# Optimization experiments

Measured on AMD Instinct MI355X. Metric: run time of the kernel, lower is better.

Reference implementation:

```python
import jax, jax.numpy as jnp
import numpy as np

HID = 64

def _lstm_layer(x_seq, h0, c0, w_ih, w_hh, b_ih, b_hh):
    # x_seq: [B,T,I]; PyTorch gate order: i, f, g, o
    x_proj = jnp.einsum('bti,gi->btg', x_seq, w_ih) + b_ih  # [B,T,4H]
    x_proj = jnp.swapaxes(x_proj, 0, 1)                      # [T,B,4H]

    def step(carry, xp):
        h, c = carry
        gates = xp + h @ w_hh.T + b_hh
        i, f, g, o = jnp.split(gates, 4, axis=-1)
        c_new = jax.nn.sigmoid(f) * c + jax.nn.sigmoid(i) * jnp.tanh(g)
        h_new = jax.nn.sigmoid(o) * jnp.tanh(c_new)
        return (h_new, c_new), h_new

    (hT, cT), hs = jax.lax.scan(step, (h0, c0), x_proj)
    return jnp.swapaxes(hs, 0, 1), hT, cT  # [B,T,H]


def setup_inputs() -> dict:
    key = jax.random.key(0)
    ks = jax.random.split(key, 12)
    B, T, I = 1024, 512, 5
    s = 1.0 / np.sqrt(HID)
    u = lambda k, shape: jax.random.uniform(k, shape, jnp.float32, -s, s)
    return {
        'x': jax.random.normal(ks[0], (B, T, I), jnp.float32),
        'h0': jnp.zeros((2, B, HID), jnp.float32),
        'c0': jnp.zeros((2, B, HID), jnp.float32),
        'w_ih0': u(ks[1], (4 * HID, I)),
        'w_hh0': u(ks[2], (4 * HID, HID)),
        'b_ih0': u(ks[3], (4 * HID,)),
        'b_hh0': u(ks[4], (4 * HID,)),
        'w_ih1': u(ks[5], (4 * HID, HID)),
        'w_hh1': u(ks[6], (4 * HID, HID)),
        'b_ih1': u(ks[7], (4 * HID,)),
        'b_hh1': u(ks[8], (4 * HID,)),
        'w_mean': u(ks[9], (1, HID)),
        'b_mean': u(ks[10], (1,)),
        'w_critic': u(ks[11], (1, HID)),
        'b_critic': jnp.zeros((1,), jnp.float32),
    }


def reference(x, h0, c0, w_ih0, w_hh0, b_ih0, b_hh0,
              w_ih1, w_hh1, b_ih1, b_hh1,
              w_mean, b_mean, w_critic, b_critic):
    out0, _, _ = _lstm_layer(x, h0[0], c0[0], w_ih0, w_hh0, b_ih0, b_hh0)
    out1, _, _ = _lstm_layer(out0, h0[1], c0[1], w_ih1, w_hh1, b_ih1, b_hh1)
    last = out1[:, -1, :]                       # [B,H]
    mean_lin = last @ w_mean.T + b_mean         # [B,1]
    mean = 2.0 * jnp.tanh(mean_lin)
    log_std = jax.nn.softplus(mean_lin)         # source bug: reuses actor_mean_fc
    state_value = last @ w_critic.T + b_critic  # [B,1]
    return mean, log_std, state_value
```

## Files before the change

kernel.cpp:

```cpp
#include <hip/hip_runtime.h>
#include <math.h>

#define NB    256
#define NT    512
#define ROWS  4
#define B_TOT 1024
#define T_TOT 512
#define HROW  104
#define XT    32

typedef _Float16 f16;
typedef _Float16 f16x8 __attribute__((ext_vector_type(8)));
typedef float    f32x4 __attribute__((ext_vector_type(4)));

__device__ __forceinline__ float rcp_f(float v){ return __builtin_amdgcn_rcpf(v); }
__device__ __forceinline__ float sig_f(float x){ return rcp_f(1.0f + __expf(-x)); }
__device__ __forceinline__ float tanh_f(float x){ return 1.0f - 2.0f*rcp_f(__expf(2.0f*x) + 1.0f); }

#define MFMA16(a,b,c) __builtin_amdgcn_mfma_f32_16x16x32_f16((a),(b),(c),0,0,0)

__global__ __launch_bounds__(NT, 2) void lstm_pipe(
    const float* __restrict__ x,
    const float* __restrict__ h0i, const float* __restrict__ c0i,
    const float* __restrict__ wih0, const float* __restrict__ whh0,
    const float* __restrict__ bih0, const float* __restrict__ bhh0,
    const float* __restrict__ wih1, const float* __restrict__ whh1,
    const float* __restrict__ bih1, const float* __restrict__ bhh1,
    const float* __restrict__ wmean, const float* __restrict__ bmean,
    const float* __restrict__ wcrit, const float* __restrict__ bcrit,
    float* __restrict__ out)
{
    const int tid  = threadIdx.x;
    const int lane = tid & 63;
    const int wv   = tid >> 6;
    const bool isX = (wv < 4);
    const int ug   = wv & 3;
    const int l15  = lane & 15;
    const int kgrp = lane >> 4;
    const int r0   = blockIdx.x * ROWS;
    const int uloc = lane >> 2;
    const int bb   = lane & 3;

    __shared__ __align__(16) f16 hbuf[2][16][HROW];
    __shared__ __align__(16) f16 ybuf[2][16][HROW];
    __shared__ float xt[ROWS][XT][5];
    __shared__ __align__(16) float gbuf[8][4][4][16];

    f16x8 aX[4][3];
    f16x8 aY[4][4];
    float bpk[4];
    float cOwn;

    if (isX){
#pragma unroll
        for (int q = 0; q < 4; ++q){
            const int gr = q*64 + ug*16 + l15;
#pragma unroll
            for (int c2 = 0; c2 < 2; ++c2){
                const float* pw = whh0 + (size_t)gr*64 + c2*32 + kgrp*8;
                f16x8 v;
#pragma unroll
                for (int j = 0; j < 8; ++j) v[j] = (f16)pw[j];
                aX[q][c2] = v;
            }
            {
                f16x8 v;
#pragma unroll
                for (int j = 0; j < 8; ++j){
                    int k = kgrp*8 + j;
                    v[j] = (k < 5) ? (f16)wih0[gr*5 + k] : (f16)0.f;
                }
                aX[q][2] = v;
            }
            const int gu = q*64 + ug*16 + uloc;
            bpk[q] = bih0[gu] + bhh0[gu];
        }
        cOwn = c0i[(size_t)(r0+bb)*64 + ug*16 + uloc];
    } else {
#pragma unroll
        for (int q = 0; q < 4; ++q){
            const int gr = q*64 + ug*16 + l15;
#pragma unroll
            for (int c2 = 0; c2 < 2; ++c2){
                const float* pw = wih1 + (size_t)gr*64 + c2*32 + kgrp*8;
                const float* qw = whh1 + (size_t)gr*64 + c2*32 + kgrp*8;
                f16x8 v, u2;
#pragma unroll
                for (int j = 0; j < 8; ++j){ v[j] = (f16)pw[j]; u2[j] = (f16)qw[j]; }
                aY[q][c2]   = v;
                aY[q][2+c2] = u2;
            }
            const int gu = q*64 + ug*16 + uloc;
            bpk[q] = bih1[gu] + bhh1[gu];
        }
        cOwn = c0i[(size_t)B_TOT*64 + (size_t)(r0+bb)*64 + ug*16 + uloc];
    }

    for (int e = tid; e < 2*16*HROW; e += NT){
        ((f16*)hbuf)[e] = (f16)0.f;
        ((f16*)ybuf)[e] = (f16)0.f;
    }
    __syncthreads();
    if (tid < ROWS*64){
        int cc = tid >> 6, u = tid & 63;
        hbuf[0][cc][u] = (f16)h0i[(size_t)(r0+cc)*64 + u];
        ybuf[1][cc][u] = (f16)h0i[(size_t)B_TOT*64 + (size_t)(r0+cc)*64 + u];
    }
    if (tid < ROWS*5){
        int cc = tid/5, i = tid - cc*5;
        hbuf[0][cc][64+i] = (f16)x[(size_t)(r0+cc)*T_TOT*5 + i];
    }
    for (int e = tid; e < ROWS*XT*5; e += NT){
        int r = e/160, rem = e - r*160, ts = rem/5, i = rem - ts*5;
        xt[r][ts][i] = x[((size_t)(r0+r)*T_TOT + ts)*5 + i];
    }
    __syncthreads();

#pragma unroll 1
    for (int t = 0; t <= T_TOT; ++t){
        const int p = t & 1;

        if ((t+1) < T_TOT && ((t+1) & 31) == 0){
            for (int e = tid; e < ROWS*XT*5; e += NT){
                int r = e/160, rem = e - r*160, ts = rem/5, i = rem - ts*5;
                xt[r][ts][i] = x[((size_t)(r0+r)*T_TOT + (t+1+ts))*5 + i];
            }
            __syncthreads();
        }
        if ((t+1) < T_TOT && tid < ROWS*5){
            int cc = tid/5, i = tid - cc*5;
            hbuf[p^1][cc][64+i] = (f16)xt[cc][(t+1)&31][i];
        }

        if (isX){ if (t < T_TOT){
            const f16* bp = &hbuf[p][l15][kgrp*8];
            f16x8 b0 = *(const f16x8*)(bp);
            f16x8 b1 = *(const f16x8*)(bp + 32);
            f16x8 b2 = *(const f16x8*)(bp + 64);
#pragma unroll
            for (int q = 0; q < 4; ++q){
                f32x4 a = {0.f,0.f,0.f,0.f};
                a = MFMA16(aX[q][0], b0, a);
                a = MFMA16(aX[q][1], b1, a);
                a = MFMA16(aX[q][2], b2, a);
                if (l15 < ROWS) *(f32x4*)&gbuf[wv][q][l15][kgrp*4] = a;
            }
            float ii = gbuf[wv][0][bb][uloc] + bpk[0];
            float ff = gbuf[wv][1][bb][uloc] + bpk[1];
            float gg = gbuf[wv][2][bb][uloc] + bpk[2];
            float oo = gbuf[wv][3][bb][uloc] + bpk[3];
            cOwn = sig_f(ff)*cOwn + sig_f(ii)*tanh_f(gg);
            hbuf[p^1][bb][ug*16 + uloc] = (f16)(sig_f(oo)*tanh_f(cOwn));
        }} else { if (t >= 1){
            const f16* hp = &hbuf[p][l15][kgrp*8];
            f16x8 b0 = *(const f16x8*)(hp);
            f16x8 b1 = *(const f16x8*)(hp + 32);
            const f16* yp = &ybuf[p][l15][kgrp*8];
            f16x8 b2 = *(const f16x8*)(yp);
            f16x8 b3 = *(const f16x8*)(yp + 32);
#pragma unroll
            for (int q = 0; q < 4; ++q){
                f32x4 a = {0.f,0.f,0.f,0.f};
                a = MFMA16(aY[q][0], b0, a);
                a = MFMA16(aY[q][1], b1, a);
                a = MFMA16(aY[q][2], b2, a);
                a = MFMA16(aY[q][3], b3, a);
                if (l15 < ROWS) *(f32x4*)&gbuf[wv][q][l15][kgrp*4] = a;
            }
            float ii = gbuf[wv][0][bb][uloc] + bpk[0];
            float ff = gbuf[wv][1][bb][uloc] + bpk[1];
            float gg = gbuf[wv][2][bb][uloc] + bpk[2];
            float oo = gbuf[wv][3][bb][uloc] + bpk[3];
            cOwn = sig_f(ff)*cOwn + sig_f(ii)*tanh_f(gg);
            ybuf[p^1][bb][ug*16 + uloc] = (f16)(sig_f(oo)*tanh_f(cOwn));
        }}
        __syncthreads();
    }

    if (wv < ROWS){
        const int cc = wv, u = lane;
        float hr = (float)ybuf[1][cc][u];
        float pm = hr * wmean[u];
        float pc = hr * wcrit[u];
#pragma unroll
        for (int o = 32; o > 0; o >>= 1){
            pm += __shfl_down(pm, o);
            pc += __shfl_down(pc, o);
        }
        if (u == 0){
            float m = pm + bmean[0];
            out[r0+cc]           = 2.f*tanh_f(m);
            out[B_TOT + r0+cc]   = __logf(1.f + __expf(m));
            out[2*B_TOT + r0+cc] = pc + bcrit[0];
        }
    }
}

extern "C" void kernel_launch(void* const* d_in, const int* in_sizes, int n_in,
                              void* d_out, int out_size, void* d_ws, size_t ws_size,
                              hipStream_t stream) {
    const float* x     = (const float*)d_in[0];
    const float* h0i   = (const float*)d_in[1];
    const float* c0i   = (const float*)d_in[2];
    const float* wih0  = (const float*)d_in[3];
    const float* whh0  = (const float*)d_in[4];
    const float* bih0  = (const float*)d_in[5];
    const float* bhh0  = (const float*)d_in[6];
    const float* wih1  = (const float*)d_in[7];
    const float* whh1  = (const float*)d_in[8];
    const float* bih1  = (const float*)d_in[9];
    const float* bhh1  = (const float*)d_in[10];
    const float* wmean = (const float*)d_in[11];
    const float* bmean = (const float*)d_in[12];
    const float* wcrit = (const float*)d_in[13];
    const float* bcrit = (const float*)d_in[14];

    lstm_pipe<<<NB, NT, 0, stream>>>(x, h0i, c0i, wih0, whh0, bih0, bhh0,
                                     wih1, whh1, bih1, bhh1,
                                     wmean, bmean, wcrit, bcrit,
                                     (float*)d_out);
}
```

Baseline: 350.5 us.

## Transpose MFMA operands and redistribute gates via shuffles instead of LDS

Swaps the MFMA operand roles so the hidden state becomes the A operand and weights the B operand, which puts batch rows on the output's row axis and hidden units on its columns. Each lane can then collect its four gate values with cross-lane shuffles from the accumulator rather than writing them to a shared-memory staging buffer and reading them back. The bias is folded into the accumulator initialisation. This removes an LDS round trip per gate per timestep on the serial critical path, at the cost of 16 shuffles plus selects per step.

```diff
diff --git a/kernel.cpp b/kernel.cpp
--- a/kernel.cpp
+++ b/kernel.cpp
@@ -19,7 +19,7 @@
 
 #define MFMA16(a,b,c) __builtin_amdgcn_mfma_f32_16x16x32_f16((a),(b),(c),0,0,0)
 
-__global__ __launch_bounds__(NT, 2) void lstm_pipe(
+__global__ __launch_bounds__(NT, 2) void lstm_tr(
     const float* __restrict__ x,
     const float* __restrict__ h0i, const float* __restrict__ c0i,
     const float* __restrict__ wih0, const float* __restrict__ whh0,
@@ -38,30 +38,27 @@
     const int l15  = lane & 15;
     const int kgrp = lane >> 4;
     const int r0   = blockIdx.x * ROWS;
-    const int uloc = lane >> 2;
-    const int bb   = lane & 3;
+    const int un   = ug*16 + l15;
 
     __shared__ __align__(16) f16 hbuf[2][16][HROW];
     __shared__ __align__(16) f16 ybuf[2][16][HROW];
     __shared__ float xt[ROWS][XT][5];
-    __shared__ __align__(16) float gbuf[8][4][4][16];
-
-    f16x8 aX[4][3];
-    f16x8 aY[4][4];
-    float bpk[4];
+
+    f16x8 bfr[4][4];
+    float bq[4];
     float cOwn;
 
     if (isX){
 #pragma unroll
         for (int q = 0; q < 4; ++q){
-            const int gr = q*64 + ug*16 + l15;
+            const int gr = q*64 + un;
 #pragma unroll
             for (int c2 = 0; c2 < 2; ++c2){
                 const float* pw = whh0 + (size_t)gr*64 + c2*32 + kgrp*8;
                 f16x8 v;
 #pragma unroll
                 for (int j = 0; j < 8; ++j) v[j] = (f16)pw[j];
-                aX[q][c2] = v;
+                bfr[q][c2] = v;
             }
             {
                 f16x8 v;
@@ -70,16 +67,16 @@
                     int k = kgrp*8 + j;
                     v[j] = (k < 5) ? (f16)wih0[gr*5 + k] : (f16)0.f;
                 }
-                aX[q][2] = v;
-            }
-            const int gu = q*64 + ug*16 + uloc;
-            bpk[q] = bih0[gu] + bhh0[gu];
-        }
-        cOwn = c0i[(size_t)(r0+bb)*64 + ug*16 + uloc];
+                bfr[q][2] = v;
+            }
+            bfr[q][3] = (f16x8)(f16)0.f;
+            bq[q] = bih0[gr] + bhh0[gr];
+        }
+        cOwn = c0i[(size_t)(r0+kgrp)*64 + un];
     } else {
 #pragma unroll
         for (int q = 0; q < 4; ++q){
-            const int gr = q*64 + ug*16 + l15;
+            const int gr = q*64 + un;
 #pragma unroll
             for (int c2 = 0; c2 < 2; ++c2){
                 const float* pw = wih1 + (size_t)gr*64 + c2*32 + kgrp*8;
@@ -87,13 +84,12 @@
                 f16x8 v, u2;
 #pragma unroll
                 for (int j = 0; j < 8; ++j){ v[j] = (f16)pw[j]; u2[j] = (f16)qw[j]; }
-                aY[q][c2]   = v;
-                aY[q][2+c2] = u2;
-            }
-            const int gu = q*64 + ug*16 + uloc;
-            bpk[q] = bih1[gu] + bhh1[gu];
-        }
-        cOwn = c0i[(size_t)B_TOT*64 + (size_t)(r0+bb)*64 + ug*16 + uloc];
+                bfr[q][c2]   = v;
+                bfr[q][2+c2] = u2;
+            }
+            bq[q] = bih1[gr] + bhh1[gr];
+        }
+        cOwn = c0i[(size_t)B_TOT*64 + (size_t)(r0+kgrp)*64 + un];
     }
 
     for (int e = tid; e < 2*16*HROW; e += NT){
@@ -111,7 +107,7 @@
         hbuf[0][cc][64+i] = (f16)x[(size_t)(r0+cc)*T_TOT*5 + i];
     }
     for (int e = tid; e < ROWS*XT*5; e += NT){
-        int r = e/160, rem = e - r*160, ts = rem/5, i = rem - ts*5;
+        int r = e/(XT*5), rem = e - r*(XT*5), ts = rem/5, i = rem - ts*5;
         xt[r][ts][i] = x[((size_t)(r0+r)*T_TOT + ts)*5 + i];
     }
     __syncthreads();
@@ -122,7 +118,7 @@
 
         if ((t+1) < T_TOT && ((t+1) & 31) == 0){
             for (int e = tid; e < ROWS*XT*5; e += NT){
-                int r = e/160, rem = e - r*160, ts = rem/5, i = rem - ts*5;
+                int r = e/(XT*5), rem = e - r*(XT*5), ts = rem/5, i = rem - ts*5;
                 xt[r][ts][i] = x[((size_t)(r0+r)*T_TOT + (t+1+ts))*5 + i];
             }
             __syncthreads();
@@ -133,46 +129,60 @@
         }
 
         if (isX){ if (t < T_TOT){
-            const f16* bp = &hbuf[p][l15][kgrp*8];
-            f16x8 b0 = *(const f16x8*)(bp);
-            f16x8 b1 = *(const f16x8*)(bp + 32);
-            f16x8 b2 = *(const f16x8*)(bp + 64);
-#pragma unroll
-            for (int q = 0; q < 4; ++q){
-                f32x4 a = {0.f,0.f,0.f,0.f};
-                a = MFMA16(aX[q][0], b0, a);
-                a = MFMA16(aX[q][1], b1, a);
-                a = MFMA16(aX[q][2], b2, a);
-                if (l15 < ROWS) *(f32x4*)&gbuf[wv][q][l15][kgrp*4] = a;
-            }
-            float ii = gbuf[wv][0][bb][uloc] + bpk[0];
-            float ff = gbuf[wv][1][bb][uloc] + bpk[1];
-            float gg = gbuf[wv][2][bb][uloc] + bpk[2];
-            float oo = gbuf[wv][3][bb][uloc] + bpk[3];
-            cOwn = sig_f(ff)*cOwn + sig_f(ii)*tanh_f(gg);
-            hbuf[p^1][bb][ug*16 + uloc] = (f16)(sig_f(oo)*tanh_f(cOwn));
+            const f16* ap = &hbuf[p][l15][kgrp*8];
+            f16x8 a0 = *(const f16x8*)(ap);
+            f16x8 a1 = *(const f16x8*)(ap + 32);
+            f16x8 a2 = *(const f16x8*)(ap + 64);
+            f32x4 ac[4];
+#pragma unroll
+            for (int q = 0; q < 4; ++q){
+                f32x4 a = {bq[q], bq[q], bq[q], bq[q]};
+                a = MFMA16(a0, bfr[q][0], a);
+                a = MFMA16(a1, bfr[q][1], a);
+                a = MFMA16(a2, bfr[q][2], a);
+                ac[q] = a;
+            }
+            float g[4];
+#pragma unroll
+            for (int q = 0; q < 4; ++q){
+                float t0 = __shfl(ac[q][0], l15);
+                float t1 = __shfl(ac[q][1], l15);
+                float t2 = __shfl(ac[q][2], l15);
+                float t3 = __shfl(ac[q][3], l15);
+                g[q] = (kgrp==0) ? t0 : (kgrp==1) ? t1 : (kgrp==2) ? t2 : t3;
+            }
+            cOwn = sig_f(g[1])*cOwn + sig_f(g[0])*tanh_f(g[2]);
+            float hn = sig_f(g[3])*tanh_f(cOwn);
+            hbuf[p^1][kgrp][un] = (f16)hn;
         }} else { if (t >= 1){
             const f16* hp = &hbuf[p][l15][kgrp*8];
-            f16x8 b0 = *(const f16x8*)(hp);
-            f16x8 b1 = *(const f16x8*)(hp + 32);
+            f16x8 a0 = *(const f16x8*)(hp);
+            f16x8 a1 = *(const f16x8*)(hp + 32);
             const f16* yp = &ybuf[p][l15][kgrp*8];
-            f16x8 b2 = *(const f16x8*)(yp);
-            f16x8 b3 = *(const f16x8*)(yp + 32);
-#pragma unroll
-            for (int q = 0; q < 4; ++q){
-                f32x4 a = {0.f,0.f,0.f,0.f};
-                a = MFMA16(aY[q][0], b0, a);
-                a = MFMA16(aY[q][1], b1, a);
-                a = MFMA16(aY[q][2], b2, a);
-                a = MFMA16(aY[q][3], b3, a);
-                if (l15 < ROWS) *(f32x4*)&gbuf[wv][q][l15][kgrp*4] = a;
-            }
-            float ii = gbuf[wv][0][bb][uloc] + bpk[0];
-            float ff = gbuf[wv][1][bb][uloc] + bpk[1];
-            float gg = gbuf[wv][2][bb][uloc] + bpk[2];
-            float oo = gbuf[wv][3][bb][uloc] + bpk[3];
-            cOwn = sig_f(ff)*cOwn + sig_f(ii)*tanh_f(gg);
-            ybuf[p^1][bb][ug*16 + uloc] = (f16)(sig_f(oo)*tanh_f(cOwn));
+            f16x8 a2 = *(const f16x8*)(yp);
+            f16x8 a3 = *(const f16x8*)(yp + 32);
+            f32x4 ac[4];
+#pragma unroll
+            for (int q = 0; q < 4; ++q){
+                f32x4 a = {bq[q], bq[q], bq[q], bq[q]};
+                a = MFMA16(a0, bfr[q][0], a);
+                a = MFMA16(a1, bfr[q][1], a);
+                a = MFMA16(a2, bfr[q][2], a);
+                a = MFMA16(a3, bfr[q][3], a);
+                ac[q] = a;
+            }
+            float g[4];
+#pragma unroll
+            for (int q = 0; q < 4; ++q){
+                float t0 = __shfl(ac[q][0], l15);
+                float t1 = __shfl(ac[q][1], l15);
+                float t2 = __shfl(ac[q][2], l15);
+                float t3 = __shfl(ac[q][3], l15);
+                g[q] = (kgrp==0) ? t0 : (kgrp==1) ? t1 : (kgrp==2) ? t2 : t3;
+            }
+            cOwn = sig_f(g[1])*cOwn + sig_f(g[0])*tanh_f(g[2]);
+            float hn = sig_f(g[3])*tanh_f(cOwn);
+            ybuf[p^1][kgrp][un] = (f16)hn;
         }}
         __syncthreads();
     }
@@ -215,8 +225,8 @@
     const float* wcrit = (const float*)d_in[13];
     const float* bcrit = (const float*)d_in[14];
 
-    lstm_pipe<<<NB, NT, 0, stream>>>(x, h0i, c0i, wih0, whh0, bih0, bhh0,
-                                     wih1, whh1, bih1, bhh1,
-                                     wmean, bmean, wcrit, bcrit,
-                                     (float*)d_out);
+    lstm_tr<<<NB, NT, 0, stream>>>(x, h0i, c0i, wih0, whh0, bih0, bhh0,
+                                   wih1, whh1, bih1, bhh1,
+                                   wmean, bmean, wcrit, bcrit,
+                                   (float*)d_out);
 }
```

Measured after the change: 390.8 us. +11.5%, slower.

## Halve block to four waves, each wave computing two unit groups

Applied to the files above, without the earlier changes.

The block shrinks from eight waves to four. Each wave now holds weight fragments for two 16-unit groups and computes both gate sets sequentially, which halves the threads taking part in each per-step barrier. Wave priority is raised around the recurrent compute. The cost is twice the serial MFMA and activation work per wave on the critical path of each timestep, plus doubled register pressure for the weight fragments.

```diff
diff --git a/kernel.cpp b/kernel.cpp
--- a/kernel.cpp
+++ b/kernel.cpp
@@ -2,7 +2,7 @@
 #include <math.h>
 
 #define NB    256
-#define NT    512
+#define NT    256
 #define ROWS  4
 #define B_TOT 1024
 #define T_TOT 512
@@ -19,7 +19,7 @@
 
 #define MFMA16(a,b,c) __builtin_amdgcn_mfma_f32_16x16x32_f16((a),(b),(c),0,0,0)
 
-__global__ __launch_bounds__(NT, 2) void lstm_pipe(
+__global__ __launch_bounds__(NT, 2) void lstm_pipe2(
     const float* __restrict__ x,
     const float* __restrict__ h0i, const float* __restrict__ c0i,
     const float* __restrict__ wih0, const float* __restrict__ whh0,
@@ -33,8 +33,8 @@
     const int tid  = threadIdx.x;
     const int lane = tid & 63;
     const int wv   = tid >> 6;
-    const bool isX = (wv < 4);
-    const int ug   = wv & 3;
+    const bool isX = (wv < 2);
+    const int wq   = wv & 1;
     const int l15  = lane & 15;
     const int kgrp = lane >> 4;
     const int r0   = blockIdx.x * ROWS;
@@ -44,56 +44,64 @@
     __shared__ __align__(16) f16 hbuf[2][16][HROW];
     __shared__ __align__(16) f16 ybuf[2][16][HROW];
     __shared__ float xt[ROWS][XT][5];
-    __shared__ __align__(16) float gbuf[8][4][4][16];
-
-    f16x8 aX[4][3];
-    f16x8 aY[4][4];
-    float bpk[4];
-    float cOwn;
+    __shared__ __align__(16) float gbuf[4][2][4][ROWS][16];
+
+    f16x8 afr[2][4][4];
+    float bpk[2][4];
+    float cOwn[2];
 
     if (isX){
 #pragma unroll
-        for (int q = 0; q < 4; ++q){
-            const int gr = q*64 + ug*16 + l15;
-#pragma unroll
-            for (int c2 = 0; c2 < 2; ++c2){
-                const float* pw = whh0 + (size_t)gr*64 + c2*32 + kgrp*8;
-                f16x8 v;
-#pragma unroll
-                for (int j = 0; j < 8; ++j) v[j] = (f16)pw[j];
-                aX[q][c2] = v;
-            }
-            {
-                f16x8 v;
-#pragma unroll
-                for (int j = 0; j < 8; ++j){
-                    int k = kgrp*8 + j;
-                    v[j] = (k < 5) ? (f16)wih0[gr*5 + k] : (f16)0.f;
-                }
-                aX[q][2] = v;
-            }
-            const int gu = q*64 + ug*16 + uloc;
-            bpk[q] = bih0[gu] + bhh0[gu];
-        }
-        cOwn = c0i[(size_t)(r0+bb)*64 + ug*16 + uloc];
+        for (int sg = 0; sg < 2; ++sg){
+            const int ug = 2*wq + sg;
+#pragma unroll
+            for (int q = 0; q < 4; ++q){
+                const int gr = q*64 + ug*16 + l15;
+#pragma unroll
+                for (int c2 = 0; c2 < 2; ++c2){
+                    const float* pw = whh0 + (size_t)gr*64 + c2*32 + kgrp*8;
+                    f16x8 v;
+#pragma unroll
+                    for (int j = 0; j < 8; ++j) v[j] = (f16)pw[j];
+                    afr[sg][q][c2] = v;
+                }
+                {
+                    f16x8 v;
+#pragma unroll
+                    for (int j = 0; j < 8; ++j){
+                        int k = kgrp*8 + j;
+                        v[j] = (k < 5) ? (f16)wih0[gr*5 + k] : (f16)0.f;
+                    }
+                    afr[sg][q][2] = v;
+                }
+                afr[sg][q][3] = (f16x8)(f16)0.f;
+                const int gu = q*64 + ug*16 + uloc;
+                bpk[sg][q] = bih0[gu] + bhh0[gu];
+            }
+            cOwn[sg] = c0i[(size_t)(r0 + bb)*64 + ug*16 + uloc];
+        }
     } else {
 #pragma unroll
-        for (int q = 0; q < 4; ++q){
-            const int gr = q*64 + ug*16 + l15;
-#pragma unroll
-            for (int c2 = 0; c2 < 2; ++c2){
-                const float* pw = wih1 + (size_t)gr*64 + c2*32 + kgrp*8;
-                const float* qw = whh1 + (size_t)gr*64 + c2*32 + kgrp*8;
-                f16x8 v, u2;
-#pragma unroll
-                for (int j = 0; j < 8; ++j){ v[j] = (f16)pw[j]; u2[j] = (f16)qw[j]; }
-                aY[q][c2]   = v;
-                aY[q][2+c2] = u2;
-            }
-            const int gu = q*64 + ug*16 + uloc;
-            bpk[q] = bih1[gu] + bhh1[gu];
-        }
-        cOwn = c0i[(size_t)B_TOT*64 + (size_t)(r0+bb)*64 + ug*16 + uloc];
+        for (int sg = 0; sg < 2; ++sg){
+            const int ug = 2*wq + sg;
+#pragma unroll
+            for (int q = 0; q < 4; ++q){
+                const int gr = q*64 + ug*16 + l15;
+#pragma unroll
+                for (int c2 = 0; c2 < 2; ++c2){
+                    const float* pw = wih1 + (size_t)gr*64 + c2*32 + kgrp*8;
+                    const float* qw = whh1 + (size_t)gr*64 + c2*32 + kgrp*8;
+                    f16x8 v, u2;
+#pragma unroll
+                    for (int j = 0; j < 8; ++j){ v[j] = (f16)pw[j]; u2[j] = (f16)qw[j]; }
+                    afr[sg][q][c2]   = v;
+                    afr[sg][q][2+c2] = u2;
+                }
+                const int gu = q*64 + ug*16 + uloc;
+                bpk[sg][q] = bih1[gu] + bhh1[gu];
+            }
+            cOwn[sg] = c0i[(size_t)B_TOT*64 + (size_t)(r0 + bb)*64 + ug*16 + uloc];
+        }
     }
 
     for (int e = tid; e < 2*16*HROW; e += NT){
@@ -111,7 +119,7 @@
         hbuf[0][cc][64+i] = (f16)x[(size_t)(r0+cc)*T_TOT*5 + i];
     }
     for (int e = tid; e < ROWS*XT*5; e += NT){
-        int r = e/160, rem = e - r*160, ts = rem/5, i = rem - ts*5;
+        int r = e/(XT*5), rem = e - r*(XT*5), ts = rem/5, i = rem - ts*5;
         xt[r][ts][i] = x[((size_t)(r0+r)*T_TOT + ts)*5 + i];
     }
     __syncthreads();
@@ -122,7 +130,7 @@
 
         if ((t+1) < T_TOT && ((t+1) & 31) == 0){
             for (int e = tid; e < ROWS*XT*5; e += NT){
-                int r = e/160, rem = e - r*160, ts = rem/5, i = rem - ts*5;
+                int r = e/(XT*5), rem = e - r*(XT*5), ts = rem/5, i = rem - ts*5;
                 xt[r][ts][i] = x[((size_t)(r0+r)*T_TOT + (t+1+ts))*5 + i];
             }
             __syncthreads();
@@ -133,46 +141,56 @@
         }
 
         if (isX){ if (t < T_TOT){
+            __builtin_amdgcn_s_setprio(1);
             const f16* bp = &hbuf[p][l15][kgrp*8];
             f16x8 b0 = *(const f16x8*)(bp);
             f16x8 b1 = *(const f16x8*)(bp + 32);
             f16x8 b2 = *(const f16x8*)(bp + 64);
 #pragma unroll
-            for (int q = 0; q < 4; ++q){
-                f32x4 a = {0.f,0.f,0.f,0.f};
-                a = MFMA16(aX[q][0], b0, a);
-                a = MFMA16(aX[q][1], b1, a);
-                a = MFMA16(aX[q][2], b2, a);
-                if (l15 < ROWS) *(f32x4*)&gbuf[wv][q][l15][kgrp*4] = a;
-            }
-            float ii = gbuf[wv][0][bb][uloc] + bpk[0];
-            float ff = gbuf[wv][1][bb][uloc] + bpk[1];
-            float gg = gbuf[wv][2][bb][uloc] + bpk[2];
-            float oo = gbuf[wv][3][bb][uloc] + bpk[3];
-            cOwn = sig_f(ff)*cOwn + sig_f(ii)*tanh_f(gg);
-            hbuf[p^1][bb][ug*16 + uloc] = (f16)(sig_f(oo)*tanh_f(cOwn));
+            for (int sg = 0; sg < 2; ++sg){
+#pragma unroll
+                for (int q = 0; q < 4; ++q){
+                    f32x4 a = {0.f,0.f,0.f,0.f};
+                    a = MFMA16(afr[sg][q][0], b0, a);
+                    a = MFMA16(afr[sg][q][1], b1, a);
+                    a = MFMA16(afr[sg][q][2], b2, a);
+                    if (l15 < ROWS) *(f32x4*)&gbuf[wv][sg][q][l15][kgrp*4] = a;
+                }
+                float gi = gbuf[wv][sg][0][bb][uloc] + bpk[sg][0];
+                float gf = gbuf[wv][sg][1][bb][uloc] + bpk[sg][1];
+                float gg = gbuf[wv][sg][2][bb][uloc] + bpk[sg][2];
+                float go = gbuf[wv][sg][3][bb][uloc] + bpk[sg][3];
+                cOwn[sg] = sig_f(gf)*cOwn[sg] + sig_f(gi)*tanh_f(gg);
+                hbuf[p^1][bb][(2*wq+sg)*16 + uloc] = (f16)(sig_f(go)*tanh_f(cOwn[sg]));
+            }
+            __builtin_amdgcn_s_setprio(0);
         }} else { if (t >= 1){
+            __builtin_amdgcn_s_setprio(1);
             const f16* hp = &hbuf[p][l15][kgrp*8];
             f16x8 b0 = *(const f16x8*)(hp);
             f16x8 b1 = *(const f16x8*)(hp + 32);
             const f16* yp = &ybuf[p][l15][kgrp*8];
-            f16x8 b2 = *(const f16x8*)(yp);
-            f16x8 b3 = *(const f16x8*)(yp + 32);
-#pragma unroll
-            for (int q = 0; q < 4; ++q){
-                f32x4 a = {0.f,0.f,0.f,0.f};
-                a = MFMA16(aY[q][0], b0, a);
-                a = MFMA16(aY[q][1], b1, a);
-                a = MFMA16(aY[q][2], b2, a);
-                a = MFMA16(aY[q][3], b3, a);
-                if (l15 < ROWS) *(f32x4*)&gbuf[wv][q][l15][kgrp*4] = a;
-            }
-            float ii = gbuf[wv][0][bb][uloc] + bpk[0];
-            float ff = gbuf[wv][1][bb][uloc] + bpk[1];
-            float gg = gbuf[wv][2][bb][uloc] + bpk[2];
-            float oo = gbuf[wv][3][bb][uloc] + bpk[3];
-            cOwn = sig_f(ff)*cOwn + sig_f(ii)*tanh_f(gg);
-            ybuf[p^1][bb][ug*16 + uloc] = (f16)(sig_f(oo)*tanh_f(cOwn));
+            f16x8 y0 = *(const f16x8*)(yp);
+            f16x8 y1 = *(const f16x8*)(yp + 32);
+#pragma unroll
+            for (int sg = 0; sg < 2; ++sg){
+#pragma unroll
+                for (int q = 0; q < 4; ++q){
+                    f32x4 a = {0.f,0.f,0.f,0.f};
+                    a = MFMA16(afr[sg][q][0], b0, a);
+                    a = MFMA16(afr[sg][q][1], b1, a);
+                    a = MFMA16(afr[sg][q][2], y0, a);
+                    a = MFMA16(afr[sg][q][3], y1, a);
+                    if (l15 < ROWS) *(f32x4*)&gbuf[wv][sg][q][l15][kgrp*4] = a;
+                }
+                float gi = gbuf[wv][sg][0][bb][uloc] + bpk[sg][0];
+                float gf = gbuf[wv][sg][1][bb][uloc] + bpk[sg][1];
+                float gg = gbuf[wv][sg][2][bb][uloc] + bpk[sg][2];
+                float go = gbuf[wv][sg][3][bb][uloc] + bpk[sg][3];
+                cOwn[sg] = sig_f(gf)*cOwn[sg] + sig_f(gi)*tanh_f(gg);
+                ybuf[p^1][bb][(2*wq+sg)*16 + uloc] = (f16)(sig_f(go)*tanh_f(cOwn[sg]));
+            }
+            __builtin_amdgcn_s_setprio(0);
         }}
         __syncthreads();
     }
@@ -215,8 +233,8 @@
     const float* wcrit = (const float*)d_in[13];
     const float* bcrit = (const float*)d_in[14];
 
-    lstm_pipe<<<NB, NT, 0, stream>>>(x, h0i, c0i, wih0, whh0, bih0, bhh0,
-                                     wih1, whh1, bih1, bhh1,
-                                     wmean, bmean, wcrit, bcrit,
-                                     (float*)d_out);
+    lstm_pipe2<<<NB, NT, 0, stream>>>(x, h0i, c0i, wih0, whh0, bih0, bhh0,
+                                      wih1, whh1, bih1, bhh1,
+                                      wmean, bmean, wcrit, bcrit,
+                                      (float*)d_out);
 }
```

Result: slower. 465.3 us (+32.7%).

## Redistribute gate rows so DPP row-shares replace LDS gate exchange

Applied to the files above, without the earlier changes.

Reorders the MFMA A-operand rows so that the four gates for each (batch,unit) pair sit in the same 16-lane row group. A thread can then collect its i/f/g/o values with DPP row_share moves instead of writing accumulators to a shared gbuf and reading them back. Biases are folded into the MFMA accumulator init, and s_setprio brackets the recurrent step. The goal is to remove an LDS round trip and its wait from the serial per-timestep critical path, at the cost of extra DPP moves and selects.

```diff
diff --git a/kernel.cpp b/kernel.cpp
--- a/kernel.cpp
+++ b/kernel.cpp
@@ -17,9 +17,15 @@
 __device__ __forceinline__ float sig_f(float x){ return rcp_f(1.0f + __expf(-x)); }
 __device__ __forceinline__ float tanh_f(float x){ return 1.0f - 2.0f*rcp_f(__expf(2.0f*x) + 1.0f); }
 
+template<int CTRL>
+__device__ __forceinline__ float dpp_mov(float v){
+    int r = __builtin_amdgcn_update_dpp(0, __float_as_int(v), CTRL, 0xF, 0xF, false);
+    return __int_as_float(r);
+}
+
 #define MFMA16(a,b,c) __builtin_amdgcn_mfma_f32_16x16x32_f16((a),(b),(c),0,0,0)
 
-__global__ __launch_bounds__(NT, 2) void lstm_pipe(
+__global__ __launch_bounds__(NT, 2) void lstm_dpp(
     const float* __restrict__ x,
     const float* __restrict__ h0i, const float* __restrict__ c0i,
     const float* __restrict__ wih0, const float* __restrict__ whh0,
@@ -34,34 +40,35 @@
     const int lane = tid & 63;
     const int wv   = tid >> 6;
     const bool isX = (wv < 4);
-    const int ug   = wv & 3;
+    const int w    = wv & 3;
     const int l15  = lane & 15;
     const int kgrp = lane >> 4;
     const int r0   = blockIdx.x * ROWS;
-    const int uloc = lane >> 2;
-    const int bb   = lane & 3;
+    const int gA   = l15 & 3;
+    const int usA  = l15 >> 2;
+    const int grp  = l15 >> 2;
+    const int bown = l15 & 3;
+    const int uown = 16*w + 4*grp + kgrp;
 
     __shared__ __align__(16) f16 hbuf[2][16][HROW];
     __shared__ __align__(16) f16 ybuf[2][16][HROW];
     __shared__ float xt[ROWS][XT][5];
-    __shared__ __align__(16) float gbuf[8][4][4][16];
-
-    f16x8 aX[4][3];
-    f16x8 aY[4][4];
-    float bpk[4];
+
+    f16x8 afr[4][4];
+    f32x4 bv[4];
     float cOwn;
 
     if (isX){
 #pragma unroll
-        for (int q = 0; q < 4; ++q){
-            const int gr = q*64 + ug*16 + l15;
+        for (int s = 0; s < 4; ++s){
+            const int gr = gA*64 + 16*w + 4*s + usA;
 #pragma unroll
             for (int c2 = 0; c2 < 2; ++c2){
                 const float* pw = whh0 + (size_t)gr*64 + c2*32 + kgrp*8;
                 f16x8 v;
 #pragma unroll
                 for (int j = 0; j < 8; ++j) v[j] = (f16)pw[j];
-                aX[q][c2] = v;
+                afr[s][c2] = v;
             }
             {
                 f16x8 v;
@@ -70,16 +77,20 @@
                     int k = kgrp*8 + j;
                     v[j] = (k < 5) ? (f16)wih0[gr*5 + k] : (f16)0.f;
                 }
-                aX[q][2] = v;
-            }
-            const int gu = q*64 + ug*16 + uloc;
-            bpk[q] = bih0[gu] + bhh0[gu];
-        }
-        cOwn = c0i[(size_t)(r0+bb)*64 + ug*16 + uloc];
+                afr[s][2] = v;
+            }
+            afr[s][3] = (f16x8)(f16)0.f;
+            const int us = 16*w + 4*s + kgrp;
+            f32x4 bb;
+#pragma unroll
+            for (int r = 0; r < 4; ++r) bb[r] = bih0[r*64 + us] + bhh0[r*64 + us];
+            bv[s] = bb;
+        }
+        cOwn = c0i[(size_t)(r0 + bown)*64 + uown];
     } else {
 #pragma unroll
-        for (int q = 0; q < 4; ++q){
-            const int gr = q*64 + ug*16 + l15;
+        for (int s = 0; s < 4; ++s){
+            const int gr = gA*64 + 16*w + 4*s + usA;
 #pragma unroll
             for (int c2 = 0; c2 < 2; ++c2){
                 const float* pw = wih1 + (size_t)gr*64 + c2*32 + kgrp*8;
@@ -87,13 +98,16 @@
                 f16x8 v, u2;
 #pragma unroll
                 for (int j = 0; j < 8; ++j){ v[j] = (f16)pw[j]; u2[j] = (f16)qw[j]; }
-                aY[q][c2]   = v;
-                aY[q][2+c2] = u2;
-            }
-            const int gu = q*64 + ug*16 + uloc;
-            bpk[q] = bih1[gu] + bhh1[gu];
-        }
-        cOwn = c0i[(size_t)B_TOT*64 + (size_t)(r0+bb)*64 + ug*16 + uloc];
+                afr[s][c2]   = v;
+                afr[s][2+c2] = u2;
+            }
+            const int us = 16*w + 4*s + kgrp;
+            f32x4 bb;
+#pragma unroll
+            for (int r = 0; r < 4; ++r) bb[r] = bih1[r*64 + us] + bhh1[r*64 + us];
+            bv[s] = bb;
+        }
+        cOwn = c0i[(size_t)B_TOT*64 + (size_t)(r0 + bown)*64 + uown];
     }
 
     for (int e = tid; e < 2*16*HROW; e += NT){
@@ -111,7 +125,7 @@
         hbuf[0][cc][64+i] = (f16)x[(size_t)(r0+cc)*T_TOT*5 + i];
     }
     for (int e = tid; e < ROWS*XT*5; e += NT){
-        int r = e/160, rem = e - r*160, ts = rem/5, i = rem - ts*5;
+        int r = e/(XT*5), rem = e - r*(XT*5), ts = rem/5, i = rem - ts*5;
         xt[r][ts][i] = x[((size_t)(r0+r)*T_TOT + ts)*5 + i];
     }
     __syncthreads();
@@ -122,7 +136,7 @@
 
         if ((t+1) < T_TOT && ((t+1) & 31) == 0){
             for (int e = tid; e < ROWS*XT*5; e += NT){
-                int r = e/160, rem = e - r*160, ts = rem/5, i = rem - ts*5;
+                int r = e/(XT*5), rem = e - r*(XT*5), ts = rem/5, i = rem - ts*5;
                 xt[r][ts][i] = x[((size_t)(r0+r)*T_TOT + (t+1+ts))*5 + i];
             }
             __syncthreads();
@@ -133,46 +147,61 @@
         }
 
         if (isX){ if (t < T_TOT){
+            __builtin_amdgcn_s_setprio(1);
             const f16* bp = &hbuf[p][l15][kgrp*8];
             f16x8 b0 = *(const f16x8*)(bp);
             f16x8 b1 = *(const f16x8*)(bp + 32);
             f16x8 b2 = *(const f16x8*)(bp + 64);
-#pragma unroll
-            for (int q = 0; q < 4; ++q){
-                f32x4 a = {0.f,0.f,0.f,0.f};
-                a = MFMA16(aX[q][0], b0, a);
-                a = MFMA16(aX[q][1], b1, a);
-                a = MFMA16(aX[q][2], b2, a);
-                if (l15 < ROWS) *(f32x4*)&gbuf[wv][q][l15][kgrp*4] = a;
-            }
-            float ii = gbuf[wv][0][bb][uloc] + bpk[0];
-            float ff = gbuf[wv][1][bb][uloc] + bpk[1];
-            float gg = gbuf[wv][2][bb][uloc] + bpk[2];
-            float oo = gbuf[wv][3][bb][uloc] + bpk[3];
-            cOwn = sig_f(ff)*cOwn + sig_f(ii)*tanh_f(gg);
-            hbuf[p^1][bb][ug*16 + uloc] = (f16)(sig_f(oo)*tanh_f(cOwn));
+            f32x4 a0 = bv[0], a1 = bv[1], a2 = bv[2], a3 = bv[3];
+            a0 = MFMA16(afr[0][0], b0, a0); a0 = MFMA16(afr[0][1], b1, a0); a0 = MFMA16(afr[0][2], b2, a0);
+            a1 = MFMA16(afr[1][0], b0, a1); a1 = MFMA16(afr[1][1], b1, a1); a1 = MFMA16(afr[1][2], b2, a1);
+            a2 = MFMA16(afr[2][0], b0, a2); a2 = MFMA16(afr[2][1], b1, a2); a2 = MFMA16(afr[2][2], b2, a2);
+            a3 = MFMA16(afr[3][0], b0, a3); a3 = MFMA16(afr[3][1], b1, a3); a3 = MFMA16(afr[3][2], b2, a3);
+            float g0, g1, g2, g3;
+            {
+                float s10 = dpp_mov<0x114>(a1[0]), s20 = dpp_mov<0x118>(a2[0]), s30 = dpp_mov<0x11C>(a3[0]);
+                float s11 = dpp_mov<0x114>(a1[1]), s21 = dpp_mov<0x118>(a2[1]), s31 = dpp_mov<0x11C>(a3[1]);
+                float s12 = dpp_mov<0x114>(a1[2]), s22 = dpp_mov<0x118>(a2[2]), s32 = dpp_mov<0x11C>(a3[2]);
+                float s13 = dpp_mov<0x114>(a1[3]), s23 = dpp_mov<0x118>(a2[3]), s33 = dpp_mov<0x11C>(a3[3]);
+                g0 = (grp==0)?a0[0]:(grp==1)?s10:(grp==2)?s20:s30;
+                g1 = (grp==0)?a0[1]:(grp==1)?s11:(grp==2)?s21:s31;
+                g2 = (grp==0)?a0[2]:(grp==1)?s12:(grp==2)?s22:s32;
+                g3 = (grp==0)?a0[3]:(grp==1)?s13:(grp==2)?s23:s33;
+            }
+            cOwn = sig_f(g1)*cOwn + sig_f(g0)*tanh_f(g2);
+            hbuf[p^1][bown][uown] = (f16)(sig_f(g3)*tanh_f(cOwn));
+            __builtin_amdgcn_s_setprio(0);
         }} else { if (t >= 1){
+            __builtin_amdgcn_s_setprio(1);
             const f16* hp = &hbuf[p][l15][kgrp*8];
             f16x8 b0 = *(const f16x8*)(hp);
             f16x8 b1 = *(const f16x8*)(hp + 32);
             const f16* yp = &ybuf[p][l15][kgrp*8];
-            f16x8 b2 = *(const f16x8*)(yp);
-            f16x8 b3 = *(const f16x8*)(yp + 32);
-#pragma unroll
-            for (int q = 0; q < 4; ++q){
-                f32x4 a = {0.f,0.f,0.f,0.f};
-                a = MFMA16(aY[q][0], b0, a);
-                a = MFMA16(aY[q][1], b1, a);
-                a = MFMA16(aY[q][2], b2, a);
-                a = MFMA16(aY[q][3], b3, a);
-                if (l15 < ROWS) *(f32x4*)&gbuf[wv][q][l15][kgrp*4] = a;
-            }
-            float ii = gbuf[wv][0][bb][uloc] + bpk[0];
-            float ff = gbuf[wv][1][bb][uloc] + bpk[1];
-            float gg = gbuf[wv][2][bb][uloc] + bpk[2];
-            float oo = gbuf[wv][3][bb][uloc] + bpk[3];
-            cOwn = sig_f(ff)*cOwn + sig_f(ii)*tanh_f(gg);
-            ybuf[p^1][bb][ug*16 + uloc] = (f16)(sig_f(oo)*tanh_f(cOwn));
+            f16x8 y0 = *(const f16x8*)(yp);
+            f16x8 y1 = *(const f16x8*)(yp + 32);
+            f32x4 a0 = bv[0], a1 = bv[1], a2 = bv[2], a3 = bv[3];
+            a0 = MFMA16(afr[0][0], b0, a0); a0 = MFMA16(afr[0][1], b1, a0);
+            a0 = MFMA16(afr[0][2], y0, a0); a0 = MFMA16(afr[0][3], y1, a0);
+            a1 = MFMA16(afr[1][0], b0, a1); a1 = MFMA16(afr[1][1], b1, a1);
+            a1 = MFMA16(afr[1][2], y0, a1); a1 = MFMA16(afr[1][3], y1, a1);
+            a2 = MFMA16(afr[2][0], b0, a2); a2 = MFMA16(afr[2][1], b1, a2);
+            a2 = MFMA16(afr[2][2], y0, a2); a2 = MFMA16(afr[2][3], y1, a2);
+            a3 = MFMA16(afr[3][0], b0, a3); a3 = MFMA16(afr[3][1], b1, a3);
+            a3 = MFMA16(afr[3][2], y0, a3); a3 = MFMA16(afr[3][3], y1, a3);
+            float g0, g1, g2, g3;
+            {
+                float s10 = dpp_mov<0x114>(a1[0]), s20 = dpp_mov<0x118>(a2[0]), s30 = dpp_mov<0x11C>(a3[0]);
+                float s11 = dpp_mov<0x114>(a1[1]), s21 = dpp_mov<0x118>(a2[1]), s31 = dpp_mov<0x11C>(a3[1]);
+                float s12 = dpp_mov<0x114>(a1[2]), s22 = dpp_mov<0x118>(a2[2]), s32 = dpp_mov<0x11C>(a3[2]);
+                float s13 = dpp_mov<0x114>(a1[3]), s23 = dpp_mov<0x118>(a2[3]), s33 = dpp_mov<0x11C>(a3[3]);
+                g0 = (grp==0)?a0[0]:(grp==1)?s10:(grp==2)?s20:s30;
+                g1 = (grp==0)?a0[1]:(grp==1)?s11:(grp==2)?s21:s31;
+                g2 = (grp==0)?a0[2]:(grp==1)?s12:(grp==2)?s22:s32;
+                g3 = (grp==0)?a0[3]:(grp==1)?s13:(grp==2)?s23:s33;
+            }
+            cOwn = sig_f(g1)*cOwn + sig_f(g0)*tanh_f(g2);
+            ybuf[p^1][bown][uown] = (f16)(sig_f(g3)*tanh_f(cOwn));
+            __builtin_amdgcn_s_setprio(0);
         }}
         __syncthreads();
     }
@@ -215,8 +244,8 @@
     const float* wcrit = (const float*)d_in[13];
     const float* bcrit = (const float*)d_in[14];
 
-    lstm_pipe<<<NB, NT, 0, stream>>>(x, h0i, c0i, wih0, whh0, bih0, bhh0,
-                                     wih1, whh1, bih1, bhh1,
-                                     wmean, bmean, wcrit, bcrit,
-                                     (float*)d_out);
+    lstm_dpp<<<NB, NT, 0, stream>>>(x, h0i, c0i, wih0, whh0, bih0, bhh0,
+                                    wih1, whh1, bih1, bhh1,
+                                    wmean, bmean, wcrit, bcrit,
+                                    (float*)d_out);
 }
```

Result: no change. 355.4 us (+1.4%).
